# Optimization experiments

Hardware: AMD Instinct MI355X
Metric: run time of the kernel (lower is better)

The kernel has to match this reference:

```python
import jax, jax.numpy as jnp
import numpy as np
import math

B, S, D, H = 16, 1024, 768, 12
Dh = D // H  # 64


def setup_inputs() -> dict:
    key = jax.random.key(0)
    ks = jax.random.split(key, 9)
    scale = 1.0 / math.sqrt(D)
    X = jax.random.normal(ks[0], (B, S, D), dtype=jnp.float32)
    # Per-head Q/K/V projections stacked along head dim: [H, D, Dh]
    Wq = jax.random.normal(ks[1], (H, D, Dh), dtype=jnp.float32) * scale
    Wk = jax.random.normal(ks[2], (H, D, Dh), dtype=jnp.float32) * scale
    Wv = jax.random.normal(ks[3], (H, D, Dh), dtype=jnp.float32) * scale
    bq = jax.random.normal(ks[4], (H, Dh), dtype=jnp.float32) * scale
    bk = jax.random.normal(ks[5], (H, Dh), dtype=jnp.float32) * scale
    bv = jax.random.normal(ks[6], (H, Dh), dtype=jnp.float32) * scale
    Wo = jax.random.normal(ks[7], (D, D), dtype=jnp.float32) * scale
    bo = jax.random.normal(ks[8], (D,), dtype=jnp.float32) * scale
    return {"X": X, "Wq": Wq, "bq": bq, "Wk": Wk, "bk": bk,
            "Wv": Wv, "bv": bv, "Wo": Wo, "bo": bo}


def reference(X, Wq, bq, Wk, bk, Wv, bv, Wo, bo):
    # Batched multi-head QKV projections (equivalent to the per-head Linear loop).
    Q = jnp.einsum('bsd,hde->bhse', X, Wq) + bq[None, :, None, :]
    K = jnp.einsum('bsd,hde->bhse', X, Wk) + bk[None, :, None, :]
    V = jnp.einsum('bsd,hde->bhse', X, Wv) + bv[None, :, None, :]
    scores = jnp.einsum('bhse,bhte->bhst', Q, K) / jnp.sqrt(jnp.float32(Dh))
    A = jax.nn.softmax(scores, axis=-1)            # [B,H,S,S]
    O = jnp.einsum('bhst,bhte->bhse', A, V)        # [B,H,S,Dh]
    # Concat heads along feature dim (matches torch cat order: head 0 first).
    msa = jnp.transpose(O, (0, 2, 1, 3)).reshape(B, S, D)
    return msa @ Wo + bo
```

## Files before the change

kernel.cpp:

```cpp
#include <hip/hip_runtime.h>
#include <hip/hip_bf16.h>

#define BB 16
#define SS 1024
#define DD 768
#define HH 12
#define DH 64

typedef short short8 __attribute__((ext_vector_type(8)));
typedef float f32x4 __attribute__((ext_vector_type(4)));
typedef float f32x16 __attribute__((ext_vector_type(16)));
typedef unsigned int uv2 __attribute__((ext_vector_type(2)));

__device__ inline float b2f(unsigned short v) {
    union { unsigned int u; float f; } x; x.u = ((unsigned int)v) << 16; return x.f;
}
__device__ inline unsigned short f2b(float f) {
    unsigned int u = __float_as_uint(f);
    u += 0x7FFFu + ((u >> 16) & 1u);
    return (unsigned short)(u >> 16);
}
__device__ inline unsigned int pk2(float a, float b) {
    __hip_bfloat162 h = __float22bfloat162_rn(make_float2(a, b));
    return *(unsigned int*)&h;
}
__device__ __forceinline__ float fast_exp2(float x) {
#if __has_builtin(__builtin_amdgcn_exp2f)
    return __builtin_amdgcn_exp2f(x);
#else
    return exp2f(x);
#endif
}
__device__ inline void cvt8(unsigned short* dst, const float* src) {
    const float4 f0 = *(const float4*)src;
    const float4 f1 = *(const float4*)(src + 4);
    uint4 o;
    o.x = pk2(f0.x, f0.y);
    o.y = pk2(f0.z, f0.w);
    o.z = pk2(f1.x, f1.y);
    o.w = pk2(f1.z, f1.w);
    *(uint4*)dst = o;
}
__device__ __forceinline__ void async16(const void* g, void* l) {
    __builtin_amdgcn_global_load_lds(
        (const __attribute__((address_space(1))) void*)g,
        (__attribute__((address_space(3))) void*)l, 16, 0, 0);
}

__global__ __launch_bounds__(256) void detect_kernel(const unsigned short* __restrict__ X,
                                                     int* __restrict__ flag) {
    __shared__ int s;
    if (threadIdx.x == 0) s = 0;
    __syncthreads();
    int c = 0;
    for (int i = threadIdx.x; i < 16384; i += 256) {
        unsigned short v = X[i];
        if ((v & 0x7FFFu) >= 0x7F80u) c = 1;
    }
    if (c) s = 1;
    __syncthreads();
    if (threadIdx.x == 0) flag[0] = s;
}

__global__ __launch_bounds__(256) void prep_all(
    const void* __restrict__ Xv,
    const void* __restrict__ Wqv, const void* __restrict__ bqv,
    const void* __restrict__ Wkv, const void* __restrict__ bkv,
    const void* __restrict__ Wvv, const void* __restrict__ bvv,
    const void* __restrict__ Wov, const void* __restrict__ bov,
    const int* __restrict__ flag,
    unsigned short* __restrict__ Xb, unsigned short* __restrict__ Wc,
    unsigned short* __restrict__ Wot, unsigned short* __restrict__ bc,
    float* __restrict__ bo32)
{
    __shared__ unsigned short Ls[64][72];
    const int dt = *flag;
    const int u = threadIdx.x;
    const int bx = blockIdx.x;

    if (bx < 6144) {
        size_t base = ((size_t)bx * 256 + u) * 8;
        if (dt) cvt8(Xb + base, (const float*)Xv + base);
        else    *(uint4*)(Xb + base) = *(const uint4*)((const unsigned short*)Xv + base);
        return;
    }
    if (bx < 6720) {
        const int idx = bx - 6144;
        const int kt = idx % 12;
        const int y  = idx / 12;
        const int rk = u >> 2;
        const int e0 = (u & 3) * 16;

        const void* src; size_t srcBase;
        unsigned short* dst; int drow;
        if (y < 36) {
            int z = y / 12, h = y % 12;
            src = (z == 0) ? Wqv : (z == 1) ? Wkv : Wvv;
            srcBase = ((size_t)h * DD + kt * 64 + rk) * DH;
            dst = Wc; drow = z * 768 + h * 64;
        } else {
            int nt = y - 36;
            src = Wov;
            srcBase = (size_t)(kt * 64 + rk) * DD + nt * 64;
            dst = Wot; drow = nt * 64;
        }
#pragma unroll
        for (int ii = 0; ii < 2; ++ii) {
            int e = e0 + ii * 8;
            if (dt) {
                const float* p = (const float*)src + srcBase + e;
                float4 a = *(const float4*)p, b = *(const float4*)(p + 4);
                float v[8] = {a.x, a.y, a.z, a.w, b.x, b.y, b.z, b.w};
#pragma unroll
                for (int j = 0; j < 8; ++j) Ls[e + j][rk] = f2b(v[j]);
            } else {
                union { uint4 v; unsigned short s[8]; } t;
                t.v = *(const uint4*)((const unsigned short*)src + srcBase + e);
#pragma unroll
                for (int j = 0; j < 8; ++j) Ls[e + j][rk] = t.s[j];
            }
        }
        __syncthreads();
        const int e = u >> 2, q = u & 3;
#pragma unroll
        for (int ii = 0; ii < 2; ++ii) {
            int kk = q * 16 + ii * 8;
            *(uint4*)(dst + (size_t)(drow + e) * DD + kt * 64 + kk) = *(const uint4*)(&Ls[e][kk]);
        }
        return;
    }
    for (int n = u; n < 2304; n += 256) {
        int z = n / 768, i = n % 768;
        const void* b = (z == 0) ? bqv : (z == 1) ? bkv : bvv;
        bc[n] = dt ? f2b(((const float*)b)[i]) : ((const unsigned short*)b)[i];
    }
    for (int n = u; n < 768; n += 256)
        bo32[n] = dt ? ((const float*)bov)[n] : b2f(((const unsigned short*)bov)[n]);
}

__global__ __launch_bounds__(256) void qkv_gemm(
    const unsigned short* __restrict__ Xb,
    const unsigned short* __restrict__ Wc,
    const unsigned short* __restrict__ bc,
    unsigned short* __restrict__ Qb, unsigned short* __restrict__ Kb,
    unsigned short* __restrict__ Vtb)
{
    __shared__ __align__(16) unsigned short lds[32768];

    const int u = threadIdx.x;
    const int lane = u & 63, w = u >> 6;
    const int ln = lane & 15, quad = lane >> 4;
    const int wm = w & 1, wn = w >> 1;

    const int flat = blockIdx.y * 18 + blockIdx.x;
    const int sf   = (flat & 7) * 288 + (flat >> 3);
    const int nt0  = sf % 18;
    const int m0   = (sf / 18) << 7;
    const int n0   = nt0 << 7;
    const int z    = nt0 / 6;
    const int hpair = (nt0 % 6) * 2;

    const int rA = w * 32 + (lane >> 3);
    const int c8 = (((lane & 7) ^ (lane >> 3)) * 8);

    f32x4 acc[4][4];
#pragma unroll
    for (int i = 0; i < 4; ++i)
#pragma unroll
        for (int j = 0; j < 4; ++j) acc[i][j] = (f32x4){0.f, 0.f, 0.f, 0.f};

    const unsigned short* Ag = Xb + (size_t)(m0 + rA) * DD + c8;
    const unsigned short* Bg = Wc + (size_t)(n0 + rA) * DD + c8;

    {
        unsigned short* lA = lds + w * 2048;
        unsigned short* lB = lds + 8192 + w * 2048;
#pragma unroll
        for (int j = 0; j < 4; ++j) {
            async16(Ag + (size_t)j * 8 * DD, lA + j * 512);
            async16(Bg + (size_t)j * 8 * DD, lB + j * 512);
        }
    }
    __syncthreads();

    for (int kb = 0; kb < 12; ++kb) {
        const int cur = kb & 1;
        if (kb < 11) {
            unsigned short* lA = lds + (cur ^ 1) * 16384 + w * 2048;
            unsigned short* lB = lds + (cur ^ 1) * 16384 + 8192 + w * 2048;
            const int k0 = (kb + 1) * 64;
#pragma unroll
            for (int j = 0; j < 4; ++j) {
                async16(Ag + (size_t)j * 8 * DD + k0, lA + j * 512);
                async16(Bg + (size_t)j * 8 * DD + k0, lB + j * 512);
            }
        }
        const unsigned short* As = lds + cur * 16384;
        const unsigned short* Bs = As + 8192;
#pragma unroll
        for (int kh = 0; kh < 2; ++kh) {
            const int sx = ((kh * 4 + quad) ^ (ln & 7)) * 8;
            short8 af[4], bf[4];
#pragma unroll
            for (int t = 0; t < 4; ++t) {
                af[t] = *(const short8*)(As + (wm * 64 + t * 16 + ln) * 64 + sx);
                bf[t] = *(const short8*)(Bs + (wn * 64 + t * 16 + ln) * 64 + sx);
            }
#pragma unroll
            for (int mt = 0; mt < 4; ++mt)
#pragma unroll
                for (int nt = 0; nt < 4; ++nt)
                    acc[mt][nt] = __builtin_amdgcn_mfma_f32_16x16x32_bf16(af[mt], bf[nt], acc[mt][nt], 0, 0, 0);
        }
        __syncthreads();
    }

    float bias[4];
#pragma unroll
    for (int nt = 0; nt < 4; ++nt) bias[nt] = b2f(bc[n0 + wn * 64 + nt * 16 + ln]);

    const int b = m0 >> 10;
    if (z < 2) {
        unsigned short* O = (z == 0) ? Qb : Kb;
        const float sc = (z == 0) ? 0.180336880111120f : 1.0f;
        const int h = hpair + wn;
        const int sb = (m0 & 1023) + wm * 64;
#pragma unroll
        for (int mt = 0; mt < 4; ++mt)
#pragma unroll
            for (int r = 0; r < 4; ++r) {
                int s = sb + mt * 16 + quad * 4 + r;
                size_t rowo = ((size_t)(b * HH + h) * SS + s) * DH;
#pragma unroll
                for (int nt = 0; nt < 4; ++nt)
                    O[rowo + nt * 16 + ln] = f2b((acc[mt][nt][r] + bias[nt]) * sc);
            }
    } else {
        __syncthreads();
#pragma unroll
        for (int mt = 0; mt < 4; ++mt)
#pragma unroll
            for (int nt = 0; nt < 4; ++nt)
#pragma unroll
                for (int r = 0; r < 4; ++r)
                    lds[(wn * 64 + nt * 16 + ln) * 136 + wm * 64 + mt * 16 + quad * 4 + r] =
                        f2b(acc[mt][nt][r] + bias[nt]);
        __syncthreads();
        const int cc = u >> 1, half = u & 1;
        const int h = hpair + (cc >> 6), e = cc & 63;
        const int sb = (m0 & 1023) + half * 64;
        unsigned short* dst = Vtb + ((size_t)(b * HH + h) * DH + e) * SS + sb;
        const unsigned short* srcp = lds + cc * 136 + half * 64;
#pragma unroll
        for (int i = 0; i < 8; ++i)
            *(uint4*)(dst + i * 8) = *(const uint4*)(srcp + i * 8);
    }
}

__global__ __launch_bounds__(256, 4) void attn_kernel(
    const unsigned short* __restrict__ Kb,
    const unsigned short* __restrict__ Vtb,
    unsigned short* __restrict__ Qb)
{
    __shared__ __align__(16) unsigned short Ks[2][4096];
    __shared__ __align__(16) unsigned short Vs[2][4096];
    unsigned short* KsF = &Ks[0][0];

    const int u = threadIdx.x;
    const int flat = (blockIdx.y << 3) | blockIdx.x;
    const int swz  = (flat & 7) * 192 + (flat >> 3);
    const int s0 = (swz & 7) << 7;
    const int bh = swz >> 3;

    const int lane = u & 63, w = u >> 6;
    const int l31 = lane & 31, hi = lane >> 5;
    const int r7 = l31 & 7;

    unsigned short* Qg = Qb + ((size_t)bh * SS + s0) * DH;
    const unsigned short* Kg = Kb + (size_t)bh * SS * DH;
    const unsigned short* Vg = Vtb + (size_t)bh * DH * SS;

    const int srow = lane >> 3;
    const int cg8  = ((lane & 7) ^ srow) * 8;

    const unsigned short* kp0 = Kg + (size_t)((w * 2 + 0) * 8 + srow) * DH + cg8;
    const unsigned short* kp1 = Kg + (size_t)((w * 2 + 1) * 8 + srow) * DH + cg8;
    const unsigned short* vp0 = Vg + (size_t)((w * 2 + 0) * 8 + srow) * SS + cg8;
    const unsigned short* vp1 = Vg + (size_t)((w * 2 + 1) * 8 + srow) * SS + cg8;

#pragma unroll
    for (int j = 0; j < 4; ++j) {
        const int r0 = (w * 4 + j) * 8 + srow;
        async16(Qg + (size_t)r0 * DH + cg8, KsF + (w * 4 + j) * 512);
    }
    __syncthreads();

    short8 qf[4];
    {
        const unsigned short* qrow = KsF + (w * 32 + l31) * 64;
#pragma unroll
        for (int ke = 0; ke < 4; ++ke)
            qf[ke] = *(const short8*)(qrow + (((ke * 2 + hi) ^ r7) * 8));
    }
    __syncthreads();

    async16(kp0, &Ks[0][(w * 2 + 0) * 512]);
    async16(kp1, &Ks[0][(w * 2 + 1) * 512]);
    async16(vp0, &Vs[0][(w * 2 + 0) * 512]);
    async16(vp1, &Vs[0][(w * 2 + 1) * 512]);
    kp0 += 64 * DH; kp1 += 64 * DH; vp0 += 64; vp1 += 64;
    __syncthreads();

    short8 ones;
#pragma unroll
    for (int i = 0; i < 8; ++i) ones[i] = (short)0x3F80;

    int off[4];
#pragma unroll
    for (int x = 0; x < 4; ++x) off[x] = l31 * 64 + (((x * 2 + hi) ^ r7) * 8);

    f32x16 oA, oB, oL;
#pragma unroll
    for (int i = 0; i < 16; ++i) { oA[i] = 0.f; oB[i] = 0.f; oL[i] = 0.f; }

    for (int kt = 0; kt < 16; ++kt) {
        const int cur = kt & 1;
        if (kt < 15) {
            unsigned short* lk = &Ks[cur ^ 1][(w * 2) * 512];
            unsigned short* lv = &Vs[cur ^ 1][(w * 2) * 512];
            async16(kp0, lk);
            async16(kp1, lk + 512);
            async16(vp0, lv);
            async16(vp1, lv + 512);
            kp0 += 64 * DH; kp1 += 64 * DH; vp0 += 64; vp1 += 64;
        }
        const unsigned short* kc = Ks[cur];
        const unsigned short* vc = Vs[cur];

        f32x16 sA, sB;
#pragma unroll
        for (int i = 0; i < 16; ++i) { sA[i] = 0.f; sB[i] = 0.f; }
        __builtin_amdgcn_s_setprio(1);
#pragma unroll
        for (int ke = 0; ke < 4; ++ke) {
            short8 kf0 = *(const short8*)(kc + off[ke]);
            short8 kf1 = *(const short8*)(kc + off[ke] + 2048);
            sA = __builtin_amdgcn_mfma_f32_32x32x16_bf16(kf0, qf[ke], sA, 0, 0, 0);
            sB = __builtin_amdgcn_mfma_f32_32x32x16_bf16(kf1, qf[ke], sB, 0, 0, 0);
        }
        __builtin_amdgcn_s_setprio(0);

        unsigned int W0[8], W1[8];
#pragma unroll
        for (int i = 0; i < 8; ++i) {
            W0[i] = pk2(fast_exp2(sA[2 * i]), fast_exp2(sA[2 * i + 1]));
            W1[i] = pk2(fast_exp2(sB[2 * i]), fast_exp2(sB[2 * i + 1]));
        }

        __builtin_amdgcn_s_setprio(1);
#define PV_STEP(Wt, ks) {                                                              \
        union { unsigned int wv[4]; short8 s; } pu;                                    \
        { uv2 rr = __builtin_amdgcn_permlane32_swap(Wt[4 * ((ks) & 1) + 0],            \
                                                    Wt[4 * ((ks) & 1) + 2], false, false); \
          pu.wv[0] = rr.x; pu.wv[2] = rr.y; }                                          \
        { uv2 rr = __builtin_amdgcn_permlane32_swap(Wt[4 * ((ks) & 1) + 1],            \
                                                    Wt[4 * ((ks) & 1) + 3], false, false); \
          pu.wv[1] = rr.x; pu.wv[3] = rr.y; }                                          \
        oL = __builtin_amdgcn_mfma_f32_32x32x16_bf16(ones, pu.s, oL, 0, 0, 0);         \
        short8 vf0 = *(const short8*)(vc + off[(ks)]);                                 \
        short8 vf1 = *(const short8*)(vc + off[(ks)] + 2048);                          \
        oA = __builtin_amdgcn_mfma_f32_32x32x16_bf16(vf0, pu.s, oA, 0, 0, 0);          \
        oB = __builtin_amdgcn_mfma_f32_32x32x16_bf16(vf1, pu.s, oB, 0, 0, 0); }
        PV_STEP(W0, 0)
        PV_STEP(W0, 1)
        PV_STEP(W1, 2)
        PV_STEP(W1, 3)
#undef PV_STEP
        __builtin_amdgcn_s_setprio(0);

        __syncthreads();
    }

    const float linv = 1.f / oL[0];

    unsigned short* Ob = KsF + w * 2048;
#define OSTORE(oc, et) {                                                   \
        _Pragma("unroll")                                                  \
        for (int rg = 0; rg < 4; ++rg) {                                   \
            uv2 wv;                                                        \
            wv.x = pk2(oc[rg * 4 + 0] * linv, oc[rg * 4 + 1] * linv);      \
            wv.y = pk2(oc[rg * 4 + 2] * linv, oc[rg * 4 + 3] * linv);      \
            *(uv2*)(Ob + l31 * 64 + ((((et) * 4 + rg) ^ r7) * 8) + hi * 4) = wv; \
        } }
    OSTORE(oA, 0)
    OSTORE(oB, 1)
#undef OSTORE

    const int rr2 = lane >> 1, q16 = lane & 1, rs = rr2 & 7;
    const unsigned short* orow = KsF + w * 2048 + rr2 * 64;
    unsigned short* gout = Qg + (size_t)(w * 32 + rr2) * DH;
#pragma unroll
    for (int i = 0; i < 4; ++i) {
        const int g = q16 * 4 + i;
        *(uint4*)(gout + g * 8) = *(const uint4*)(orow + ((g ^ rs) * 8));
    }
}

__global__ __launch_bounds__(256) void oproj_gemm(
    const unsigned short* __restrict__ Ob,
    const unsigned short* __restrict__ Wot,
    const float* __restrict__ bo32,
    float* __restrict__ out)
{
    __shared__ __align__(16) unsigned short lds[128 * 128];
    unsigned short* As = lds;
    unsigned short* Bs = lds + 128 * 64;

    const int u = threadIdx.x;
    const int lane = u & 63, w = u >> 6;
    const int ln = lane & 15, quad = lane >> 4;
    const int wm = w & 1, wn = w >> 1;

    const int flat = blockIdx.y * 6 + blockIdx.x;
    const int sf   = (flat & 7) * 96 + (flat >> 3);
    const int n0   = (sf % 6) << 7;
    const int m0   = (sf / 6) << 7;
    const int b = m0 >> 10, s0t = m0 & 1023;

    const int rA = w * 32 + (lane >> 3);
    const int c8 = (((lane & 7) ^ (lane >> 3)) * 8);

    f32x4 acc[4][4];
#pragma unroll
    for (int i = 0; i < 4; ++i)
#pragma unroll
        for (int j = 0; j < 4; ++j) acc[i][j] = (f32x4){0.f, 0.f, 0.f, 0.f};

    const unsigned short* Bg = Wot + (size_t)(n0 + rA) * DD + c8;
    unsigned short* lA0 = As + w * 2048;
    unsigned short* lB0 = Bs + w * 2048;

    for (int kb = 0; kb < 12; ++kb) {
        if (kb) __syncthreads();
        const unsigned short* Ag = Ob + ((size_t)(b * HH + kb) * SS + s0t + rA) * DH + c8;
#pragma unroll
        for (int j = 0; j < 4; ++j) {
            async16(Ag + (size_t)j * 8 * DH, lA0 + j * 512);
            async16(Bg + (size_t)j * 8 * DD + kb * 64, lB0 + j * 512);
        }
        __syncthreads();
#pragma unroll
        for (int kh = 0; kh < 2; ++kh) {
            const int sx = ((kh * 4 + quad) ^ (ln & 7)) * 8;
            short8 af[4], bf[4];
#pragma unroll
            for (int t = 0; t < 4; ++t) {
                af[t] = *(const short8*)(As + (wm * 64 + t * 16 + ln) * 64 + sx);
                bf[t] = *(const short8*)(Bs + (wn * 64 + t * 16 + ln) * 64 + sx);
            }
#pragma unroll
            for (int mt = 0; mt < 4; ++mt)
#pragma unroll
                for (int nt = 0; nt < 4; ++nt)
                    acc[mt][nt] = __builtin_amdgcn_mfma_f32_16x16x32_bf16(af[mt], bf[nt], acc[mt][nt], 0, 0, 0);
        }
    }

    float bias[4];
#pragma unroll
    for (int nt = 0; nt < 4; ++nt) bias[nt] = bo32[n0 + wn * 64 + nt * 16 + ln];
#pragma unroll
    for (int mt = 0; mt < 4; ++mt)
#pragma unroll
        for (int r = 0; r < 4; ++r) {
            int m = m0 + wm * 64 + mt * 16 + quad * 4 + r;
            float* orow = out + (size_t)m * DD + n0 + wn * 64;
#pragma unroll
            for (int nt = 0; nt < 4; ++nt)
                orow[nt * 16 + ln] = acc[mt][nt][r] + bias[nt];
        }
}

extern "C" void kernel_launch(void* const* d_in, const int* in_sizes, int n_in,
                              void* d_out, int out_size, void* d_ws, size_t ws_size,
                              hipStream_t stream)
{
    const void* X  = d_in[0];
    const void* Wq = d_in[1];
    const void* bq = d_in[2];
    const void* Wk = d_in[3];
    const void* bk = d_in[4];
    const void* Wv = d_in[5];
    const void* bv = d_in[6];
    const void* Wo = d_in[7];
    const void* bo = d_in[8];
    float* out = (float*)d_out;

    const size_t NE = (size_t)BB * HH * SS * DH;
    char* p = (char*)d_ws;
    int* flag = (int*)p;                 p += 256;
    unsigned short* Qb  = (unsigned short*)p;  p += NE * 2;
    unsigned short* Kb  = (unsigned short*)p;  p += NE * 2;
    unsigned short* Vtb = (unsigned short*)p;  p += NE * 2;
    unsigned short* Xb  = (unsigned short*)p;  p += (size_t)BB * SS * DD * 2;
    unsigned short* Wc  = (unsigned short*)p;  p += (size_t)3 * DD * DD * 2;
    unsigned short* Wot = (unsigned short*)p;  p += (size_t)DD * DD * 2;
    unsigned short* bcb = (unsigned short*)p;  p += 4608;
    float* bo32 = (float*)p;                   p += 3072;

    detect_kernel<<<1, 256, 0, stream>>>((const unsigned short*)X, flag);
    prep_all<<<6721, 256, 0, stream>>>(X, Wq, bq, Wk, bk, Wv, bv, Wo, bo, flag,
                                       Xb, Wc, Wot, bcb, bo32);
    qkv_gemm<<<dim3(18, 128), 256, 0, stream>>>(Xb, Wc, bcb, Qb, Kb, Vtb);
    attn_kernel<<<dim3(8, 192), 256, 0, stream>>>(Kb, Vtb, Qb);
    oproj_gemm<<<dim3(6, 128), 256, 0, stream>>>(Qb, Wot, bo32, out);
}
```

Before: 285.7 us.

## Double query rows per attention block and replace ones-MFMA row sum with VALU

Each attention block now handles 256 query rows (64 per wave, in two 32-row bands) instead of 128. Every K/V tile loaded into shared memory is therefore reused across twice as many queries, which halves K/V global traffic and the number of barriers per query. The softmax denominator is no longer computed by an extra MFMA against a ones vector. It is now accumulated with VALU adds and combined across lanes with a shuffle at the end. The cost is higher register pressure, reflected in launch bounds lowered from 4 to 3 blocks, and half as many blocks in the grid.

```diff
diff --git a/kernel.cpp b/kernel.cpp
--- a/kernel.cpp
+++ b/kernel.cpp
@@ -257,20 +257,18 @@
     }
 }
 
-__global__ __launch_bounds__(256, 4) void attn_kernel(
+__global__ __launch_bounds__(256, 3) void attn_kernel(
     const unsigned short* __restrict__ Kb,
     const unsigned short* __restrict__ Vtb,
     unsigned short* __restrict__ Qb)
 {
-    __shared__ __align__(16) unsigned short Ks[2][4096];
-    __shared__ __align__(16) unsigned short Vs[2][4096];
-    unsigned short* KsF = &Ks[0][0];
+    __shared__ __align__(16) unsigned short L[16384];
 
     const int u = threadIdx.x;
-    const int flat = (blockIdx.y << 3) | blockIdx.x;
-    const int swz  = (flat & 7) * 192 + (flat >> 3);
-    const int s0 = (swz & 7) << 7;
-    const int bh = swz >> 3;
+    const int flat = (blockIdx.y << 2) | blockIdx.x;
+    const int swz  = (flat & 7) * 96 + (flat >> 3);
+    const int s0 = (swz & 3) << 8;
+    const int bh = swz >> 2;
 
     const int lane = u & 63, w = u >> 6;
     const int l31 = lane & 31, hi = lane >> 5;
@@ -289,120 +287,138 @@
     const unsigned short* vp1 = Vg + (size_t)((w * 2 + 1) * 8 + srow) * SS + cg8;
 
 #pragma unroll
-    for (int j = 0; j < 4; ++j) {
-        const int r0 = (w * 4 + j) * 8 + srow;
-        async16(Qg + (size_t)r0 * DH + cg8, KsF + (w * 4 + j) * 512);
+    for (int j = 0; j < 8; ++j) {
+        const int r0 = (w * 8 + j) * 8 + srow;
+        async16(Qg + (size_t)r0 * DH + cg8, L + (w * 8 + j) * 512);
     }
     __syncthreads();
 
-    short8 qf[4];
-    {
-        const unsigned short* qrow = KsF + (w * 32 + l31) * 64;
+    short8 qf[2][4];
+#pragma unroll
+    for (int b = 0; b < 2; ++b) {
+        const unsigned short* qrow = L + (w * 64 + b * 32 + l31) * 64;
 #pragma unroll
         for (int ke = 0; ke < 4; ++ke)
-            qf[ke] = *(const short8*)(qrow + (((ke * 2 + hi) ^ r7) * 8));
+            qf[b][ke] = *(const short8*)(qrow + (((ke * 2 + hi) ^ r7) * 8));
     }
     __syncthreads();
 
-    async16(kp0, &Ks[0][(w * 2 + 0) * 512]);
-    async16(kp1, &Ks[0][(w * 2 + 1) * 512]);
-    async16(vp0, &Vs[0][(w * 2 + 0) * 512]);
-    async16(vp1, &Vs[0][(w * 2 + 1) * 512]);
+    async16(kp0, L + (w * 2 + 0) * 512);
+    async16(kp1, L + (w * 2 + 1) * 512);
+    async16(vp0, L + 8192 + (w * 2 + 0) * 512);
+    async16(vp1, L + 8192 + (w * 2 + 1) * 512);
     kp0 += 64 * DH; kp1 += 64 * DH; vp0 += 64; vp1 += 64;
     __syncthreads();
 
-    short8 ones;
-#pragma unroll
-    for (int i = 0; i < 8; ++i) ones[i] = (short)0x3F80;
-
     int off[4];
 #pragma unroll
     for (int x = 0; x < 4; ++x) off[x] = l31 * 64 + (((x * 2 + hi) ^ r7) * 8);
 
-    f32x16 oA, oB, oL;
-#pragma unroll
-    for (int i = 0; i < 16; ++i) { oA[i] = 0.f; oB[i] = 0.f; oL[i] = 0.f; }
+    f32x16 oA0, oB0, oA1, oB1;
+#pragma unroll
+    for (int i = 0; i < 16; ++i) { oA0[i] = 0.f; oB0[i] = 0.f; oA1[i] = 0.f; oB1[i] = 0.f; }
+    float ls0 = 0.f, ls1 = 0.f;
 
     for (int kt = 0; kt < 16; ++kt) {
         const int cur = kt & 1;
         if (kt < 15) {
-            unsigned short* lk = &Ks[cur ^ 1][(w * 2) * 512];
-            unsigned short* lv = &Vs[cur ^ 1][(w * 2) * 512];
+            unsigned short* lk = L + (cur ^ 1) * 4096 + (w * 2) * 512;
+            unsigned short* lv = L + 8192 + (cur ^ 1) * 4096 + (w * 2) * 512;
             async16(kp0, lk);
             async16(kp1, lk + 512);
             async16(vp0, lv);
             async16(vp1, lv + 512);
             kp0 += 64 * DH; kp1 += 64 * DH; vp0 += 64; vp1 += 64;
         }
-        const unsigned short* kc = Ks[cur];
-        const unsigned short* vc = Vs[cur];
-
-        f32x16 sA, sB;
-#pragma unroll
-        for (int i = 0; i < 16; ++i) { sA[i] = 0.f; sB[i] = 0.f; }
+        const unsigned short* kc = L + cur * 4096;
+        const unsigned short* vc = L + 8192 + cur * 4096;
+
+        unsigned int W0a[8], W1a[8], W0b[8], W1b[8];
+#define QK_BAND(bb, W0v, W1v, lsv) {                                                   \
+        f32x16 sA, sB;                                                                 \
+        _Pragma("unroll")                                                              \
+        for (int i = 0; i < 16; ++i) { sA[i] = 0.f; sB[i] = 0.f; }                     \
+        __builtin_amdgcn_s_setprio(1);                                                 \
+        _Pragma("unroll")                                                              \
+        for (int ke = 0; ke < 4; ++ke) {                                               \
+            short8 kf0 = *(const short8*)(kc + off[ke]);                               \
+            short8 kf1 = *(const short8*)(kc + off[ke] + 2048);                        \
+            sA = __builtin_amdgcn_mfma_f32_32x32x16_bf16(kf0, qf[bb][ke], sA, 0, 0, 0);\
+            sB = __builtin_amdgcn_mfma_f32_32x32x16_bf16(kf1, qf[bb][ke], sB, 0, 0, 0);\
+        }                                                                              \
+        __builtin_amdgcn_s_setprio(0);                                                 \
+        _Pragma("unroll")                                                              \
+        for (int i = 0; i < 8; ++i) {                                                  \
+            float a0 = fast_exp2(sA[2 * i]), b0 = fast_exp2(sA[2 * i + 1]);            \
+            float a1 = fast_exp2(sB[2 * i]), b1 = fast_exp2(sB[2 * i + 1]);            \
+            lsv += (a0 + b0) + (a1 + b1);                                              \
+            W0v[i] = pk2(a0, b0);                                                      \
+            W1v[i] = pk2(a1, b1);                                                      \
+        } }
+        QK_BAND(0, W0a, W1a, ls0)
+        QK_BAND(1, W0b, W1b, ls1)
+#undef QK_BAND
+
         __builtin_amdgcn_s_setprio(1);
-#pragma unroll
-        for (int ke = 0; ke < 4; ++ke) {
-            short8 kf0 = *(const short8*)(kc + off[ke]);
-            short8 kf1 = *(const short8*)(kc + off[ke] + 2048);
-            sA = __builtin_amdgcn_mfma_f32_32x32x16_bf16(kf0, qf[ke], sA, 0, 0, 0);
-            sB = __builtin_amdgcn_mfma_f32_32x32x16_bf16(kf1, qf[ke], sB, 0, 0, 0);
-        }
-        __builtin_amdgcn_s_setprio(0);
-
-        unsigned int W0[8], W1[8];
-#pragma unroll
-        for (int i = 0; i < 8; ++i) {
-            W0[i] = pk2(fast_exp2(sA[2 * i]), fast_exp2(sA[2 * i + 1]));
-            W1[i] = pk2(fast_exp2(sB[2 * i]), fast_exp2(sB[2 * i + 1]));
-        }
-
-        __builtin_amdgcn_s_setprio(1);
-#define PV_STEP(Wt, ks) {                                                              \
-        union { unsigned int wv[4]; short8 s; } pu;                                    \
-        { uv2 rr = __builtin_amdgcn_permlane32_swap(Wt[4 * ((ks) & 1) + 0],            \
-                                                    Wt[4 * ((ks) & 1) + 2], false, false); \
+#define MKPU(Wt0, Wt1, ks, pu) {                                                       \
+        const unsigned int* Wsel = ((ks) < 2) ? Wt0 : Wt1;                             \
+        { uv2 rr = __builtin_amdgcn_permlane32_swap(Wsel[4 * ((ks) & 1) + 0],          \
+                                                    Wsel[4 * ((ks) & 1) + 2], false, false); \
           pu.wv[0] = rr.x; pu.wv[2] = rr.y; }                                          \
-        { uv2 rr = __builtin_amdgcn_permlane32_swap(Wt[4 * ((ks) & 1) + 1],            \
-                                                    Wt[4 * ((ks) & 1) + 3], false, false); \
-          pu.wv[1] = rr.x; pu.wv[3] = rr.y; }                                          \
-        oL = __builtin_amdgcn_mfma_f32_32x32x16_bf16(ones, pu.s, oL, 0, 0, 0);         \
+        { uv2 rr = __builtin_amdgcn_permlane32_swap(Wsel[4 * ((ks) & 1) + 1],          \
+                                                    Wsel[4 * ((ks) & 1) + 3], false, false); \
+          pu.wv[1] = rr.x; pu.wv[3] = rr.y; } }
+#define PV_STEP(ks) {                                                                  \
         short8 vf0 = *(const short8*)(vc + off[(ks)]);                                 \
         short8 vf1 = *(const short8*)(vc + off[(ks)] + 2048);                          \
-        oA = __builtin_amdgcn_mfma_f32_32x32x16_bf16(vf0, pu.s, oA, 0, 0, 0);          \
-        oB = __builtin_amdgcn_mfma_f32_32x32x16_bf16(vf1, pu.s, oB, 0, 0, 0); }
-        PV_STEP(W0, 0)
-        PV_STEP(W0, 1)
-        PV_STEP(W1, 2)
-        PV_STEP(W1, 3)
+        union { unsigned int wv[4]; short8 s; } pa, pb;                                \
+        MKPU(W0a, W1a, (ks), pa)                                                       \
+        MKPU(W0b, W1b, (ks), pb)                                                       \
+        oA0 = __builtin_amdgcn_mfma_f32_32x32x16_bf16(vf0, pa.s, oA0, 0, 0, 0);        \
+        oB0 = __builtin_amdgcn_mfma_f32_32x32x16_bf16(vf1, pa.s, oB0, 0, 0, 0);        \
+        oA1 = __builtin_amdgcn_mfma_f32_32x32x16_bf16(vf0, pb.s, oA1, 0, 0, 0);        \
+        oB1 = __builtin_amdgcn_mfma_f32_32x32x16_bf16(vf1, pb.s, oB1, 0, 0, 0); }
+        PV_STEP(0)
+        PV_STEP(1)
+        PV_STEP(2)
+        PV_STEP(3)
 #undef PV_STEP
+#undef MKPU
         __builtin_amdgcn_s_setprio(0);
 
         __syncthreads();
     }
 
-    const float linv = 1.f / oL[0];
-
-    unsigned short* Ob = KsF + w * 2048;
-#define OSTORE(oc, et) {                                                   \
-        _Pragma("unroll")                                                  \
-        for (int rg = 0; rg < 4; ++rg) {                                   \
-            uv2 wv;                                                        \
-            wv.x = pk2(oc[rg * 4 + 0] * linv, oc[rg * 4 + 1] * linv);      \
-            wv.y = pk2(oc[rg * 4 + 2] * linv, oc[rg * 4 + 3] * linv);      \
-            *(uv2*)(Ob + l31 * 64 + ((((et) * 4 + rg) ^ r7) * 8) + hi * 4) = wv; \
+    float ot0 = __shfl(ls0, lane ^ 32, 64);
+    float ot1 = __shfl(ls1, lane ^ 32, 64);
+    const float inv0 = 1.f / (ls0 + ot0);
+    const float inv1 = 1.f / (ls1 + ot1);
+
+    unsigned short* Ob = L + w * 4096;
+#define OSTORE(oc, bb, et, invv) {                                          \
+        _Pragma("unroll")                                                   \
+        for (int rg = 0; rg < 4; ++rg) {                                    \
+            uv2 wv;                                                         \
+            wv.x = pk2(oc[rg * 4 + 0] * invv, oc[rg * 4 + 1] * invv);       \
+            wv.y = pk2(oc[rg * 4 + 2] * invv, oc[rg * 4 + 3] * invv);       \
+            *(uv2*)(Ob + ((bb) * 32 + l31) * 64 + ((((et) * 4 + rg) ^ r7) * 8) + hi * 4) = wv; \
         } }
-    OSTORE(oA, 0)
-    OSTORE(oB, 1)
+    OSTORE(oA0, 0, 0, inv0)
+    OSTORE(oB0, 0, 1, inv0)
+    OSTORE(oA1, 1, 0, inv1)
+    OSTORE(oB1, 1, 1, inv1)
 #undef OSTORE
 
     const int rr2 = lane >> 1, q16 = lane & 1, rs = rr2 & 7;
-    const unsigned short* orow = KsF + w * 2048 + rr2 * 64;
-    unsigned short* gout = Qg + (size_t)(w * 32 + rr2) * DH;
-#pragma unroll
-    for (int i = 0; i < 4; ++i) {
-        const int g = q16 * 4 + i;
-        *(uint4*)(gout + g * 8) = *(const uint4*)(orow + ((g ^ rs) * 8));
+#pragma unroll
+    for (int b = 0; b < 2; ++b) {
+        const unsigned short* orow = L + w * 4096 + (b * 32 + rr2) * 64;
+        unsigned short* gout = Qg + (size_t)(w * 64 + b * 32 + rr2) * DH;
+#pragma unroll
+        for (int i = 0; i < 4; ++i) {
+            const int g = q16 * 4 + i;
+            *(uint4*)(gout + g * 8) = *(const uint4*)(orow + ((g ^ rs) * 8));
+        }
     }
 }
 
@@ -512,6 +528,6 @@
     prep_all<<<6721, 256, 0, stream>>>(X, Wq, bq, Wk, bk, Wv, bv, Wo, bo, flag,
                                        Xb, Wc, Wot, bcb, bo32);
     qkv_gemm<<<dim3(18, 128), 256, 0, stream>>>(Xb, Wc, bcb, Qb, Kb, Vtb);
-    attn_kernel<<<dim3(8, 192), 256, 0, stream>>>(Kb, Vtb, Qb);
+    attn_kernel<<<dim3(4, 192), 256, 0, stream>>>(Kb, Vtb, Qb);
     oproj_gemm<<<dim3(6, 128), 256, 0, stream>>>(Qb, Wot, bo32, out);
 }
```

Result: slower. 433.8 us (+51.8%).
